# Kernel tuning notes

Hardware: AMD Instinct MI355X
Metric: run time of the kernel (lower is better)

Reference implementation:

```python
import jax, jax.numpy as jnp
import numpy as np

B, T, K, H = 8192, 96, 32, 768  # batch, max_len, output_dim (tags), bert hidden


def setup_inputs() -> dict:
    key = jax.random.key(0)
    k1, k2, k3, k4 = jax.random.split(key, 4)
    hidden = jax.random.normal(k1, (B, H), dtype=jnp.float32)
    target = jax.random.randint(k2, (B, T), 0, K, dtype=jnp.int32)
    # Dense(output_dim * max_len) params
    W = jax.random.normal(k3, (H, T * K), dtype=jnp.float32) * 0.02
    b = jnp.zeros((T * K,), dtype=jnp.float32)
    # tf.random.uniform transition matrix
    transitions = jax.random.uniform(k4, (K, K), dtype=jnp.float32)
    return {"hidden": hidden, "target": target, "W": W, "b": b, "transitions": transitions}


def _crf_log_norm(em_tm, transitions):
    # em_tm: [T, B, K] time-major emissions. Forward algorithm (logsumexp recurrence).
    def step(alpha, em_t):
        # alpha: [B, K]; broadcast over next-tag axis
        new = jax.nn.logsumexp(alpha[:, :, None] + transitions[None, :, :], axis=1) + em_t
        return new, None
    alpha, _ = jax.lax.scan(step, em_tm[0], em_tm[1:])
    return jax.nn.logsumexp(alpha, axis=-1)  # [B]


def _crf_sequence_score(em_btk, target, transitions):
    # unary: emission score at gold tags; binary: transition scores along gold path
    unary = jnp.take_along_axis(em_btk, target[..., None], axis=-1)[..., 0].sum(-1)
    binary = transitions[target[:, :-1], target[:, 1:]].sum(-1)
    return unary + binary  # [B]


def _viterbi_decode(em_tm, transitions):
    # em_tm: [T, B, K]. Max-product forward pass collecting backpointers.
    def fwd(v, em_t):
        scores = v[:, :, None] + transitions[None, :, :]  # [B, K_prev, K_next]
        bp = jnp.argmax(scores, axis=1).astype(jnp.int32)  # [B, K]
        return jnp.max(scores, axis=1) + em_t, bp
    v, bps = jax.lax.scan(fwd, em_tm[0], em_tm[1:])  # bps: [T-1, B, K]
    last_tag = jnp.argmax(v, axis=-1).astype(jnp.int32)  # [B]
    # backtrace (reverse scan); output index i is the tag at time i
    def back(tag, bp_t):
        prev = jnp.take_along_axis(bp_t, tag[:, None], axis=1)[:, 0]
        return prev, prev
    _, prevs = jax.lax.scan(back, last_tag, bps, reverse=True)  # [T-1, B]
    tags = jnp.concatenate([prevs, last_tag[None, :]], axis=0)  # [T, B]
    return jnp.transpose(tags), jnp.max(v, axis=-1)


def reference(hidden, target, W, b, transitions):
    # Dense with sigmoid, then reshape to (B, max_len, output_dim)
    em = jax.nn.sigmoid(hidden @ W + b).reshape(hidden.shape[0], T, K)
    em_tm = jnp.transpose(em, (1, 0, 2))  # time-major for scan
    log_likelihood = _crf_sequence_score(em, target, transitions) - _crf_log_norm(em_tm, transitions)
    decode_predict, _ = _viterbi_decode(em_tm, transitions)
    return decode_predict, log_likelihood
```

## Files before the change

### kernel.cpp

```cpp
#include <hip/hip_runtime.h>
#include <cstdint>
#include <cstddef>

#define B_  8192
#define T_  96
#define K_  32
#define H_  768
#define NK_ (T_ * K_)

typedef __attribute__((ext_vector_type(8))) _Float16 f16x8;
typedef __attribute__((ext_vector_type(4))) float    f32x4;

#define SCALE_UP   4096.0f
#define SCALE_DOWN (1.0f / 16777216.0f)

__device__ __forceinline__ void load_lds16(const void* g, void* l) {
    __builtin_amdgcn_global_load_lds(
        (const __attribute__((address_space(1))) unsigned int*)g,
        (__attribute__((address_space(3))) unsigned int*)l,
        16, 0, 0);
}

__global__ __launch_bounds__(256) void split_fused_kernel(
    const float* __restrict__ A, const float* __restrict__ W,
    _Float16* __restrict__ Ath, _Float16* __restrict__ Atl,
    _Float16* __restrict__ Wth, _Float16* __restrict__ Wtl)
{
    int g = blockIdx.x * 256 + threadIdx.x;
    if (g < B_ * 96) {
        const int row = g / 96;
        const int o   = g - row * 96;
        const int ks  = o >> 2, qq = o & 3;
        const int r   = row & 127, rb = row >> 7;
        const size_t dst = (size_t)(rb * 24 + ks) * 4096 + r * 32 + ((qq ^ ((r >> 1) & 3)) << 3);

        f32x4 v0 = *(const f32x4*)(A + (size_t)row * H_ + o * 8);
        f32x4 v1 = *(const f32x4*)(A + (size_t)row * H_ + o * 8 + 4);
        f16x8 hi, lo;
#pragma unroll
        for (int e = 0; e < 8; e++) {
            float x = ((e < 4) ? v0[e] : v1[e - 4]) * SCALE_UP;
            _Float16 h = (_Float16)x;
            hi[e] = h;
            lo[e] = (_Float16)(x - (float)h);
        }
        *(f16x8*)&Ath[dst] = hi;
        *(f16x8*)&Atl[dst] = lo;
    } else {
        g -= B_ * 96;
        const int ko  = g / NK_;
        const int col = g - ko * NK_;
        const int k0  = ko * 8;
        const int cb  = col >> 7, n = col & 127;
        const int ks  = k0 >> 5, qq = (k0 & 31) >> 3;
        const size_t dst = (size_t)(cb * 24 + ks) * 4096 + n * 32 + ((qq ^ ((n >> 1) & 3)) << 3);

        f16x8 hi, lo;
#pragma unroll
        for (int j = 0; j < 8; j++) {
            float x = W[(size_t)(k0 + j) * NK_ + col] * SCALE_UP;
            _Float16 h = (_Float16)x;
            hi[j] = h;
            lo[j] = (_Float16)(x - (float)h);
        }
        *(f16x8*)&Wth[dst] = hi;
        *(f16x8*)&Wtl[dst] = lo;
    }
}

__global__ __launch_bounds__(256, 2) void gemm_mfma_sigmoid_kernel(
    const _Float16* __restrict__ Ath, const _Float16* __restrict__ Atl,
    const _Float16* __restrict__ Wth, const _Float16* __restrict__ Wtl,
    const float* __restrict__ bias, float* __restrict__ em)
{
    __shared__ _Float16 lds[2][4][4096];

    const int tid  = threadIdx.x;
    const int bid  = blockIdx.x;
    const int wgid = (bid & 7) * 192 + (bid >> 3);
    const int cb   = wgid % 24;
    const int rb   = wgid / 24;
    const int lane = tid & 63;
    const int w    = tid >> 6;
    const int wr   = w >> 1, wc = w & 1;
    const int fr   = lane & 15;
    const int kg   = lane >> 4;

    const _Float16* srcs[4] = {
        Ath + (size_t)(rb * 24) * 4096, Atl + (size_t)(rb * 24) * 4096,
        Wth + (size_t)(cb * 24) * 4096, Wtl + (size_t)(cb * 24) * 4096 };

    auto stage = [&](int ks, int bb) {
#pragma unroll
        for (int m = 0; m < 4; m++) {
            const _Float16* s = srcs[m] + (size_t)ks * 4096 + w * 1024 + lane * 8;
            _Float16* d = &lds[bb][m][w * 1024];
            load_lds16(s, d);
            load_lds16(s + 512, d + 512);
        }
    };

    f32x4 acc[4][4];
#pragma unroll
    for (int i = 0; i < 4; i++)
#pragma unroll
        for (int j = 0; j < 4; j++) acc[i][j] = (f32x4)0.0f;

    int cur = 0;
    stage(0, 0);

    for (int ks = 0; ks < 24; ks++) {
        __syncthreads();
        if (ks + 1 < 24) stage(ks + 1, cur ^ 1);

        f16x8 fah[4], fal[4], fbh[4], fbl[4];
#pragma unroll
        for (int mi = 0; mi < 4; mi++) {
            const int r   = wr * 64 + mi * 16 + fr;
            const int idx = r * 32 + ((kg ^ ((r >> 1) & 3)) << 3);
            fah[mi] = *(const f16x8*)&lds[cur][0][idx];
            fal[mi] = *(const f16x8*)&lds[cur][1][idx];
        }
#pragma unroll
        for (int ni = 0; ni < 4; ni++) {
            const int r   = wc * 64 + ni * 16 + fr;
            const int idx = r * 32 + ((kg ^ ((r >> 1) & 3)) << 3);
            fbh[ni] = *(const f16x8*)&lds[cur][2][idx];
            fbl[ni] = *(const f16x8*)&lds[cur][3][idx];
        }
#pragma unroll
        for (int mi = 0; mi < 4; mi++)
#pragma unroll
            for (int ni = 0; ni < 4; ni++) {
                acc[mi][ni] = __builtin_amdgcn_mfma_f32_16x16x32_f16(fah[mi], fbh[ni], acc[mi][ni], 0, 0, 0);
                acc[mi][ni] = __builtin_amdgcn_mfma_f32_16x16x32_f16(fah[mi], fbl[ni], acc[mi][ni], 0, 0, 0);
                acc[mi][ni] = __builtin_amdgcn_mfma_f32_16x16x32_f16(fal[mi], fbh[ni], acc[mi][ni], 0, 0, 0);
            }
        cur ^= 1;
    }

    const int er = rb * 128 + wr * 64 + (lane >> 4) * 4;
    const int ec = cb * 128 + wc * 64 + fr;
#pragma unroll
    for (int ni = 0; ni < 4; ni++) {
        const int   gc = ec + ni * 16;
        const float bv = bias[gc];
#pragma unroll
        for (int mi = 0; mi < 4; mi++)
#pragma unroll
            for (int r = 0; r < 4; r++) {
                const int gr = er + mi * 16 + r;
                float x = acc[mi][ni][r] * SCALE_DOWN + bv;
                em[(size_t)gr * NK_ + gc] = 1.0f / (1.0f + __expf(-x));
            }
    }
}


#define VSTEP(T_, SH_, WI_)                                               \
  {                                                                       \
    const float cem = na; na = emb[((T_) + 1) * K_];                      \
    vxs[k] = va;                                                          \
    __builtin_amdgcn_wave_barrier();                                      \
    float bva = -1e30f; int bia = 0;                                      \
    _Pragma("unroll")                                                     \
    for (int j = 0; j < 8; j++) {                                         \
      f32x4 vq = *(const f32x4*)&vxs[4 * j];                              \
      float s0 = vq[0] + tca[4 * j];                                      \
      float s1 = vq[1] + tca[4 * j + 1];                                  \
      float s2 = vq[2] + tca[4 * j + 2];                                  \
      float s3 = vq[3] + tca[4 * j + 3];                                  \
      float w0 = (s1 > s0) ? s1 : s0;                                     \
      int   i0 = (s1 > s0) ? (4 * j + 1) : (4 * j);                       \
      float w1 = (s3 > s2) ? s3 : s2;                                     \
      int   i1 = (s3 > s2) ? (4 * j + 3) : (4 * j + 2);                   \
      if (w1 > w0) { w0 = w1; i0 = i1; }                                  \
      if (w0 > bva) { bva = w0; bia = i0; }                               \
    }                                                                     \
    va = bva + cem;                                                       \
    bpw |= (unsigned int)bia << (5 * (SH_));                              \
    if ((SH_) == 5) { bps[k * 17 + (WI_)] = bpw; bpw = 0; }               \
    __builtin_amdgcn_wave_barrier();                                      \
  }

__global__ __launch_bounds__(256, 4) void crf_roles_kernel(
    const float* __restrict__ em,
    const int* __restrict__ target,
    const float* __restrict__ trans,
    float* __restrict__ out_tags,
    float* __restrict__ ll)
{
    __shared__ float trans_s[K_ * K_];
    __shared__ float Eex[4][36];
    __shared__ float vex[4][36];
    __shared__ unsigned int bp5[4][545];
    __shared__ unsigned char tgt_s[4][T_];

    const int tid  = threadIdx.x;
    const int w    = tid >> 6;
    const int lane = tid & 63;
    const int half = lane >> 5;
    const int k    = lane & 31;
    const bool isFwd = (w < 2);
    const int s    = (((isFwd ? w : w - 2) << 1) | half);
    const int b    = blockIdx.x * 4 + s;

    for (int i = tid; i < K_ * K_; i += 256) trans_s[i] = trans[i];
    __syncthreads();

    const float* emb = em + (size_t)b * NK_ + k;

    if (isFwd) {
        float Ea2[K_];
#pragma unroll
        for (int p = 0; p < K_; p++) Ea2[p] = __expf(trans_s[p * K_ + k]);

        const int t0 = target[b * T_ + k];
        const int t1 = target[b * T_ + 32 + k];
        const int t2 = target[b * T_ + 64 + k];
        tgt_s[s][k]      = (unsigned char)t0;
        tgt_s[s][k + 32] = (unsigned char)t1;
        tgt_s[s][k + 64] = (unsigned char)t2;
        __builtin_amdgcn_wave_barrier();
        const float* emrow = em + (size_t)b * NK_;
        float gold = emrow[k * K_ + t0] + emrow[(k + 32) * K_ + t1] + emrow[(k + 64) * K_ + t2];
        if (k > 0) gold += trans_s[(int)tgt_s[s][k - 1] * K_ + t0];
        gold += trans_s[(int)tgt_s[s][k + 31] * K_ + t1];
        gold += trans_s[(int)tgt_s[s][k + 63] * K_ + t2];

        float Ea = __expf(emb[0]);
        int   expo_sum = 0;
        float na = emb[K_];
        float* exs = &Eex[s][0];

        for (int t = 1; t <= 95; ++t) {
            const float cem = na;
            na = emb[(t + 1) * K_];
            exs[k] = Ea;
            __builtin_amdgcn_wave_barrier();
            float fa = 0.0f;
#pragma unroll
            for (int j = 0; j < 8; j++) {
                f32x4 q = *(const f32x4*)&exs[4 * j];
                fa = fmaf(q[0], Ea2[4 * j],     fa);
                fa = fmaf(q[1], Ea2[4 * j + 1], fa);
                fa = fmaf(q[2], Ea2[4 * j + 2], fa);
                fa = fmaf(q[3], Ea2[4 * j + 3], fa);
            }
            Ea = fa * __expf(cem - 4.0f);
            __builtin_amdgcn_wave_barrier();

            if ((t % 12) == 0) {
                float m = Ea;
#pragma unroll
                for (int d = 16; d >= 1; d >>= 1) m = fmaxf(m, __shfl_xor(m, d));
                const unsigned int ebits = (__float_as_uint(m) >> 23) & 255u;
                const float sc = __uint_as_float((254u - ebits) << 23);
                Ea *= sc;
                expo_sum += (int)ebits - 127;
            }
        }

        float S = Ea;
#pragma unroll
        for (int d = 16; d >= 1; d >>= 1) S += __shfl_xor(S, d);
        const float logZ = __logf(S) + 380.0f + (float)expo_sum * 0.69314718055994531f;

        float gs = gold;
#pragma unroll
        for (int d = 16; d >= 1; d >>= 1) gs += __shfl_xor(gs, d);

        if (k == 0) ll[b] = gs - logZ;

    } else {
        float tca[K_];
#pragma unroll
        for (int p = 0; p < K_; p++) tca[p] = trans_s[p * K_ + k];

        float va = emb[0];
        float na = emb[K_];
        unsigned int bpw = 0;
        float* vxs = &vex[s][0];
        unsigned int* bps = &bp5[s][0];

        for (int it = 0; it < 7; ++it) {
            const int tb = it * 12 + 1;
            const int wi = it * 2;
            VSTEP(tb + 0, 0, wi)  VSTEP(tb + 1, 1, wi)  VSTEP(tb + 2, 2, wi)
            VSTEP(tb + 3, 3, wi)  VSTEP(tb + 4, 4, wi)  VSTEP(tb + 5, 5, wi)
            VSTEP(tb + 6, 0, wi + 1)  VSTEP(tb + 7, 1, wi + 1)  VSTEP(tb + 8, 2, wi + 1)
            VSTEP(tb + 9, 3, wi + 1)  VSTEP(tb + 10, 4, wi + 1) VSTEP(tb + 11, 5, wi + 1)
        }
        VSTEP(85, 0, 14) VSTEP(86, 1, 14) VSTEP(87, 2, 14)
        VSTEP(88, 3, 14) VSTEP(89, 4, 14) VSTEP(90, 5, 14)
        VSTEP(91, 0, 15) VSTEP(92, 1, 15) VSTEP(93, 2, 15)
        VSTEP(94, 3, 15) VSTEP(95, 4, 15)
        bps[k * 17 + 15] = bpw;
        __builtin_amdgcn_wave_barrier();

        float bv = va; int bi = k;
#pragma unroll
        for (int d = 16; d >= 1; d >>= 1) {
            float ov = __shfl_xor(bv, d);
            int   oi = __shfl_xor(bi, d);
            if (ov > bv || (ov == bv && oi < bi)) { bv = ov; bi = oi; }
        }

        if (k == 0) {
            float* ot = out_tags + (size_t)b * T_;
            int tag = bi;
            ot[T_ - 1] = (float)tag;
            for (int t = T_ - 2; t >= 0; t--) {
                unsigned int wd = bps[tag * 17 + t / 6];
                tag = (int)((wd >> (5 * (t % 6))) & 31u);
                ot[t] = (float)tag;
            }
        }
    }
}

extern "C" void kernel_launch(void* const* d_in, const int* in_sizes, int n_in,
                              void* d_out, int out_size, void* d_ws, size_t ws_size,
                              hipStream_t stream)
{
    const float* hidden = (const float*)d_in[0];
    const int*   target = (const int*)d_in[1];
    const float* W      = (const float*)d_in[2];
    const float* bias   = (const float*)d_in[3];
    const float* trans  = (const float*)d_in[4];

    float* out      = (float*)d_out;
    float* out_tags = out;
    float* out_ll   = out + (size_t)B_ * T_;

    char* ws = (char*)d_ws;
    const size_t emB = (size_t)B_ * NK_ * 4;
    const size_t ahB = (size_t)B_ * H_ * 2;
    const size_t whB = (size_t)H_ * NK_ * 2;

    float*    em  = (float*)ws;
    _Float16* Ath = (_Float16*)(ws + emB);
    _Float16* Atl = (_Float16*)(ws + emB + ahB);
    _Float16* Wth = (_Float16*)(ws + emB + 2 * ahB);
    _Float16* Wtl = (_Float16*)(ws + emB + 2 * ahB + whB);

    split_fused_kernel<<<(B_ * 96 + NK_ * 96) / 256, 256, 0, stream>>>(
        hidden, W, Ath, Atl, Wth, Wtl);

    gemm_mfma_sigmoid_kernel<<<1536, 256, 0, stream>>>(Ath, Atl, Wth, Wtl, bias, em);

    crf_roles_kernel<<<B_ / 4, 256, 0, stream>>>(em, target, trans, out_tags, out_ll);
}
```

Baseline: 248.9 us.

## Load A fragments directly from global in MFMA order, stage only W in LDS

The split kernel now writes the fp16 hi/lo copies of the activations in a per-wave MFMA fragment order, so each lane reads its A fragments straight from global memory with contiguous 16-byte loads. Only the W tiles are staged through LDS. This halves LDS use and lets launch bounds rise to 3 blocks per CU for more occupancy. The cost is that A reads come from global/L2 without double buffering, and the two waves sharing a row group each read the same A data separately, so load latency may be less well hidden.

```diff
diff --git a/kernel.cpp b/kernel.cpp
--- a/kernel.cpp
+++ b/kernel.cpp
@@ -30,9 +30,12 @@
     if (g < B_ * 96) {
         const int row = g / 96;
         const int o   = g - row * 96;
-        const int ks  = o >> 2, qq = o & 3;
-        const int r   = row & 127, rb = row >> 7;
-        const size_t dst = (size_t)(rb * 24 + ks) * 4096 + r * 32 + ((qq ^ ((r >> 1) & 3)) << 3);
+        const int p   = row >> 6;
+        const int mi  = (row >> 4) & 3;
+        const int fr  = row & 15;
+        const int ks  = o >> 2;
+        const int kg  = o & 3;
+        const size_t dst = ((size_t)(p * 24 + ks) * 4 + mi) * 512 + kg * 128 + fr * 8;
 
         f32x4 v0 = *(const f32x4*)(A + (size_t)row * H_ + o * 8);
         f32x4 v1 = *(const f32x4*)(A + (size_t)row * H_ + o * 8 + 4);
@@ -68,12 +71,12 @@
     }
 }
 
-__global__ __launch_bounds__(256, 2) void gemm_mfma_sigmoid_kernel(
+__global__ __launch_bounds__(256, 3) void gemm_mfma_sigmoid_kernel(
     const _Float16* __restrict__ Ath, const _Float16* __restrict__ Atl,
     const _Float16* __restrict__ Wth, const _Float16* __restrict__ Wtl,
     const float* __restrict__ bias, float* __restrict__ em)
 {
-    __shared__ _Float16 lds[2][4][4096];
+    __shared__ _Float16 lds[2][2][4096];
 
     const int tid  = threadIdx.x;
     const int bid  = blockIdx.x;
@@ -86,14 +89,15 @@
     const int fr   = lane & 15;
     const int kg   = lane >> 4;
 
-    const _Float16* srcs[4] = {
-        Ath + (size_t)(rb * 24) * 4096, Atl + (size_t)(rb * 24) * 4096,
+    const _Float16* srcB[2] = {
         Wth + (size_t)(cb * 24) * 4096, Wtl + (size_t)(cb * 24) * 4096 };
-
-    auto stage = [&](int ks, int bb) {
-#pragma unroll
-        for (int m = 0; m < 4; m++) {
-            const _Float16* s = srcs[m] + (size_t)ks * 4096 + w * 1024 + lane * 8;
+    const _Float16* aH = Ath + (size_t)((rb * 2 + wr) * 24) * 2048 + lane * 8;
+    const _Float16* aL = Atl + (size_t)((rb * 2 + wr) * 24) * 2048 + lane * 8;
+
+    auto stageB = [&](int ks, int bb) {
+#pragma unroll
+        for (int m = 0; m < 2; m++) {
+            const _Float16* s = srcB[m] + (size_t)ks * 4096 + w * 1024 + lane * 8;
             _Float16* d = &lds[bb][m][w * 1024];
             load_lds16(s, d);
             load_lds16(s + 512, d + 512);
@@ -107,26 +111,28 @@
         for (int j = 0; j < 4; j++) acc[i][j] = (f32x4)0.0f;
 
     int cur = 0;
-    stage(0, 0);
+    stageB(0, 0);
 
     for (int ks = 0; ks < 24; ks++) {
+        f16x8 fah[4], fal[4];
+        const _Float16* pH = aH + (size_t)ks * 2048;
+        const _Float16* pL = aL + (size_t)ks * 2048;
+#pragma unroll
+        for (int mi = 0; mi < 4; mi++) {
+            fah[mi] = *(const f16x8*)(pH + mi * 512);
+            fal[mi] = *(const f16x8*)(pL + mi * 512);
+        }
+
         __syncthreads();
-        if (ks + 1 < 24) stage(ks + 1, cur ^ 1);
-
-        f16x8 fah[4], fal[4], fbh[4], fbl[4];
-#pragma unroll
-        for (int mi = 0; mi < 4; mi++) {
-            const int r   = wr * 64 + mi * 16 + fr;
-            const int idx = r * 32 + ((kg ^ ((r >> 1) & 3)) << 3);
-            fah[mi] = *(const f16x8*)&lds[cur][0][idx];
-            fal[mi] = *(const f16x8*)&lds[cur][1][idx];
-        }
+        if (ks + 1 < 24) stageB(ks + 1, cur ^ 1);
+
+        f16x8 fbh[4], fbl[4];
 #pragma unroll
         for (int ni = 0; ni < 4; ni++) {
             const int r   = wc * 64 + ni * 16 + fr;
             const int idx = r * 32 + ((kg ^ ((r >> 1) & 3)) << 3);
-            fbh[ni] = *(const f16x8*)&lds[cur][2][idx];
-            fbl[ni] = *(const f16x8*)&lds[cur][3][idx];
+            fbh[ni] = *(const f16x8*)&lds[cur][0][idx];
+            fbl[ni] = *(const f16x8*)&lds[cur][1][idx];
         }
 #pragma unroll
         for (int mi = 0; mi < 4; mi++)
```

Result: slower. 256.1 us (+2.9%).
